# Kernel tuning notes

Hardware: AMD Instinct MI355X
Metric: run time of the kernel (lower is better)

The kernel has to match this reference:

```python
import jax, jax.numpy as jnp
import numpy as np


def setup_inputs() -> dict:
    key = jax.random.key(0)
    k1, k2 = jax.random.split(key)
    pred_m = jax.random.normal(k1, (64, 1, 512, 512), dtype=jnp.float32)
    # boxes: (x, y, s_x, s_y) per (batch, frame, target); values in [0, 256)
    multi_targets = jax.random.randint(k2, (64, 5, 32, 4), 0, 256, dtype=jnp.int32)
    return {"pred_m": pred_m, "multi_targets": multi_targets}


def _paint_heatmap(multi_targets, B, H, W, dtype):
    """Vectorized replacement for the triple-nested box-fill loop.

    Uses a 2D difference-array scatter + double cumsum: each box adds
    +1/-1 at its four corners; after prefix sums, count>0 marks painted
    pixels (original sets them to 255 regardless of overlap).
    """
    gt = multi_targets.reshape(B, -1, 4)  # [B, N, 4], N = n_frames*n_targets
    x, y, sx, sy = gt[..., 0], gt[..., 1], gt[..., 2], gt[..., 3]
    # python slicing clamps the end of the slice at H/W
    x1 = jnp.minimum(x, H)
    y1 = jnp.minimum(y, W)
    x2 = jnp.minimum(x + sx, H)
    y2 = jnp.minimum(y + sy, W)
    b_idx = jnp.broadcast_to(jnp.arange(B)[:, None], x.shape)
    diff = jnp.zeros((B, H + 1, W + 1), jnp.int32)
    diff = diff.at[b_idx, x1, y1].add(1)
    diff = diff.at[b_idx, x1, y2].add(-1)
    diff = diff.at[b_idx, x2, y1].add(-1)
    diff = diff.at[b_idx, x2, y2].add(1)
    count = jnp.cumsum(jnp.cumsum(diff, axis=1), axis=2)[:, :H, :W]
    return (count > 0).astype(dtype) * jnp.asarray(255.0, dtype)


def reference(pred_m, multi_targets):
    B, _, H, W = pred_m.shape
    heatmap = _paint_heatmap(multi_targets, B, H, W, pred_m.dtype)  # [B, H, W]
    target = heatmap[:, None]            # [B, 1, H, W]
    pred = jax.nn.sigmoid(pred_m)        # [B, 1, H, W]
    smooth = jnp.asarray(1.0, pred_m.dtype)
    intersection = jnp.sum(pred * target, axis=(1, 2, 3))
    pred_sum = jnp.sum(pred, axis=(1, 2, 3))
    target_sum = jnp.sum(target, axis=(1, 2, 3))
    loss = (intersection + smooth) / (pred_sum + target_sum - intersection + smooth)
    return 1.0 - jnp.mean(loss)
```

## Files before the change

### kernel.cpp

```cpp
#include <hip/hip_runtime.h>
#include <math.h>

#define SLICES 32
#define ROWS_PER_SLICE 16
#define NBOXES 160

static __device__ __forceinline__ float fast_sigmoid(float x) {
    return __builtin_amdgcn_rcpf(1.0f + __expf(-x));
}

__global__ __launch_bounds__(256) void mask_kernel(
    const int* __restrict__ targets, unsigned* __restrict__ gmask)
{
    __shared__ uint2 s_box[NBOXES];
    __shared__ int s_wcnt[4];

    const int t = threadIdx.x;
    const int slice = blockIdx.x;
    const int b = blockIdx.y;
    const int r0 = slice * ROWS_PER_SLICE;
    const int lane = t & 63, wave = t >> 6;

    bool keep = false;
    unsigned px = 0, py = 0;
    if (t < NBOXES) {
        const int4 g = ((const int4*)targets)[(size_t)b * NBOXES + t];
        int x1 = min(g.x, 512), y1 = min(g.y, 512);
        int x2 = min(g.x + g.z, 512), y2 = min(g.y + g.w, 512);
        int cx1 = max(x1, r0), cx2 = min(x2, r0 + ROWS_PER_SLICE);
        px = (unsigned)cx1 | ((unsigned)cx2 << 16);
        py = (unsigned)y1 | ((unsigned)y2 << 16);
        keep = (cx2 > cx1) && (y2 > y1);
    }
    const unsigned long long bal = __ballot(keep);
    if (lane == 0) s_wcnt[wave] = (int)__popcll(bal);
    __syncthreads();
    int wbase = 0;
    for (int w = 0; w < wave; ++w) wbase += s_wcnt[w];
    const int nb = s_wcnt[0] + s_wcnt[1] + s_wcnt[2] + s_wcnt[3];
    if (keep) {
        const int idx = wbase + (int)__popcll(bal & ((1ull << lane) - 1ull));
        s_box[idx] = make_uint2(px, py);
    }
    __syncthreads();

    const int r = r0 + (t >> 4);
    const unsigned wb = (unsigned)(t & 15) * 32u;
    unsigned m = 0;
#pragma unroll 2
    for (int k = 0; k < nb; ++k) {
        const uint2 bx = s_box[k];
        const int x1 = (int)(bx.x & 0xffffu), x2 = (int)(bx.x >> 16);
        const int y1 = (int)(bx.y & 0xffffu), y2 = (int)(bx.y >> 16);
        const bool in_row = (r >= x1) && (r < x2);
        int lo = max(y1, (int)wb), hi = min(y2, (int)wb + 32);
        int nn = hi - lo;
        unsigned bits = 0xFFFFFFFFu >> ((32 - nn) & 31);
        unsigned contrib = bits << ((unsigned)(lo - (int)wb) & 31u);
        m |= (in_row && nn > 0) ? contrib : 0u;
    }
    gmask[(size_t)b * 8192 + (size_t)r0 * 16 + t] = m;
}

__global__ __launch_bounds__(256, 4) void stream_kernel(
    const float* __restrict__ pred, const unsigned* __restrict__ gmask,
    float* __restrict__ partials)
{
    const int t = threadIdx.x;
    const int slice = blockIdx.x;
    const int b = blockIdx.y;
    const int r0 = slice * ROWS_PER_SLICE;
    const int lane = t & 63, wave = t >> 6;
    const int col4 = t & 127;
    const int rb = t >> 7;
    const int widx = col4 >> 3;
    const unsigned bb = (unsigned)(col4 & 7) * 4u;

    const unsigned* gm = gmask + (size_t)b * 8192 + (size_t)(r0 + rb) * 16 + widx;
    unsigned w0 = gm[0 * 32];
    unsigned w1 = gm[1 * 32];
    unsigned w2 = gm[2 * 32];
    unsigned w3 = gm[3 * 32];
    unsigned w4 = gm[4 * 32];
    unsigned w5 = gm[5 * 32];
    unsigned w6 = gm[6 * 32];
    unsigned w7 = gm[7 * 32];

    const float4* p4 = (const float4*)pred;
    const size_t g0 = (size_t)b * 65536 + (size_t)(r0 + rb) * 128 + col4;
    float4 v0 = p4[g0 + 0 * 256];
    float4 v1 = p4[g0 + 1 * 256];
    float4 v2 = p4[g0 + 2 * 256];
    float4 v3 = p4[g0 + 3 * 256];
    float4 v4 = p4[g0 + 4 * 256];
    float4 v5 = p4[g0 + 5 * 256];
    float4 v6 = p4[g0 + 6 * 256];
    float4 v7 = p4[g0 + 7 * 256];

    float psum = 0.0f, isum = 0.0f;
    int cnt = 0;
#define ACC(V, W)                                                       \
    {                                                                   \
        const unsigned n = ((W) >> bb) & 0xFu;                          \
        float s0 = fast_sigmoid((V).x);                                 \
        float s1 = fast_sigmoid((V).y);                                 \
        float s2 = fast_sigmoid((V).z);                                 \
        float s3 = fast_sigmoid((V).w);                                 \
        psum += (s0 + s1) + (s2 + s3);                                  \
        cnt += __popc(n);                                               \
        isum += ((n & 1u) ? s0 : 0.0f) + ((n & 2u) ? s1 : 0.0f)         \
              + ((n & 4u) ? s2 : 0.0f) + ((n & 8u) ? s3 : 0.0f);        \
    }
    ACC(v0, w0) ACC(v1, w1) ACC(v2, w2) ACC(v3, w3)
    ACC(v4, w4) ACC(v5, w5) ACC(v6, w6) ACC(v7, w7)
#undef ACC
    float csum = (float)cnt;

    for (int off = 32; off > 0; off >>= 1) {
        psum += __shfl_down(psum, off);
        isum += __shfl_down(isum, off);
        csum += __shfl_down(csum, off);
    }
    if (lane == 0) {
        float* o = partials + (((size_t)b * SLICES + slice) * 4 + wave) * 3;
        o[0] = psum; o[1] = isum; o[2] = csum;
    }
}

__global__ __launch_bounds__(64) void final_kernel(
    const float* __restrict__ partials, float* __restrict__ out)
{
    const int b = threadIdx.x;
    double P = 0, I = 0, C = 0;
    const float* p = partials + (size_t)b * SLICES * 4 * 3;
    for (int s = 0; s < SLICES * 4; ++s) {
        P += (double)p[s * 3 + 0];
        I += (double)p[s * 3 + 1];
        C += (double)p[s * 3 + 2];
    }
    const double inter = 255.0 * I;
    const double tsum  = 255.0 * C;
    double loss = (inter + 1.0) / (P + tsum - inter + 1.0);
    for (int off = 32; off > 0; off >>= 1) loss += __shfl_down(loss, off);
    if (b == 0) out[0] = (float)(1.0 - loss / 64.0);
}

extern "C" void kernel_launch(void* const* d_in, const int* in_sizes, int n_in,
                              void* d_out, int out_size, void* d_ws, size_t ws_size,
                              hipStream_t stream) {
    const float* pred    = (const float*)d_in[0];
    const int*   targets = (const int*)d_in[1];
    float* out = (float*)d_out;

    float* partials = (float*)d_ws;
    unsigned* gmask = (unsigned*)((char*)d_ws + (96 << 10));

    dim3 grid(SLICES, 64);
    mask_kernel<<<grid, 256, 0, stream>>>(targets, gmask);
    stream_kernel<<<grid, 256, 0, stream>>>(pred, gmask, partials);
    final_kernel<<<1, 64, 0, stream>>>(partials, out);
}
```

Measured before the change: 113.0 us.

## Fuse mask painting into streaming reduction with early inline-asm pred loads

Merges the mask-building kernel and the sigmoid reduction kernel into one launch. The mask is kept in shared memory instead of being written to and read back from global memory. The pred loads are issued through inline asm before the box processing, so their latency overlaps the mask computation, with an explicit s_waitcnt before use. Partials move to a structure-of-arrays layout so the final kernel can read them as float4. This removes one launch and a global round trip, but relies on hand-written waitcnt and asm loads that the compiler cannot track.

```diff
diff --git a/kernel.cpp b/kernel.cpp
--- a/kernel.cpp
+++ b/kernel.cpp
@@ -4,27 +4,46 @@
 #define SLICES 32
 #define ROWS_PER_SLICE 16
 #define NBOXES 160
+#define THREADS 256
 
 static __device__ __forceinline__ float fast_sigmoid(float x) {
     return __builtin_amdgcn_rcpf(1.0f + __expf(-x));
 }
 
-__global__ __launch_bounds__(256) void mask_kernel(
-    const int* __restrict__ targets, unsigned* __restrict__ gmask)
+__global__ __launch_bounds__(THREADS, 4) void paint_reduce_kernel(
+    const float* __restrict__ pred, const int* __restrict__ targets,
+    float* __restrict__ partials)
 {
-    __shared__ uint2 s_box[NBOXES];
-    __shared__ int s_wcnt[4];
+    __shared__ uint2 s_box[192];
+    __shared__ int s_wcnt[3];
+    __shared__ unsigned s_mask[256];
 
     const int t = threadIdx.x;
     const int slice = blockIdx.x;
     const int b = blockIdx.y;
     const int r0 = slice * ROWS_PER_SLICE;
     const int lane = t & 63, wave = t >> 6;
+    const int col4 = t & 127;
+    const int rb = t >> 7;
+
+    int4 g = make_int4(0, 0, 0, 0);
+    if (t < NBOXES) g = ((const int4*)targets)[(size_t)b * NBOXES + t];
+
+    const float4* p4 = (const float4*)pred + (size_t)b * 65536
+                     + (size_t)(r0 + rb) * 128 + col4;
+    float4 v0, v1, v2, v3, v4, v5, v6, v7;
+    asm volatile("global_load_dwordx4 %0, %1, off" : "=v"(v0) : "v"(p4 + 0 * 256));
+    asm volatile("global_load_dwordx4 %0, %1, off" : "=v"(v1) : "v"(p4 + 1 * 256));
+    asm volatile("global_load_dwordx4 %0, %1, off" : "=v"(v2) : "v"(p4 + 2 * 256));
+    asm volatile("global_load_dwordx4 %0, %1, off" : "=v"(v3) : "v"(p4 + 3 * 256));
+    asm volatile("global_load_dwordx4 %0, %1, off" : "=v"(v4) : "v"(p4 + 4 * 256));
+    asm volatile("global_load_dwordx4 %0, %1, off" : "=v"(v5) : "v"(p4 + 5 * 256));
+    asm volatile("global_load_dwordx4 %0, %1, off" : "=v"(v6) : "v"(p4 + 6 * 256));
+    asm volatile("global_load_dwordx4 %0, %1, off" : "=v"(v7) : "v"(p4 + 7 * 256));
 
     bool keep = false;
     unsigned px = 0, py = 0;
     if (t < NBOXES) {
-        const int4 g = ((const int4*)targets)[(size_t)b * NBOXES + t];
         int x1 = min(g.x, 512), y1 = min(g.y, 512);
         int x2 = min(g.x + g.z, 512), y2 = min(g.y + g.w, 512);
         int cx1 = max(x1, r0), cx2 = min(x2, r0 + ROWS_PER_SLICE);
@@ -33,69 +52,45 @@
         keep = (cx2 > cx1) && (y2 > y1);
     }
     const unsigned long long bal = __ballot(keep);
-    if (lane == 0) s_wcnt[wave] = (int)__popcll(bal);
-    __syncthreads();
-    int wbase = 0;
-    for (int w = 0; w < wave; ++w) wbase += s_wcnt[w];
-    const int nb = s_wcnt[0] + s_wcnt[1] + s_wcnt[2] + s_wcnt[3];
+    if (wave < 3 && lane == 0) s_wcnt[wave] = (int)__popcll(bal);
     if (keep) {
-        const int idx = wbase + (int)__popcll(bal & ((1ull << lane) - 1ull));
-        s_box[idx] = make_uint2(px, py);
+        const int idx = (int)__popcll(bal & ((1ull << lane) - 1ull));
+        s_box[wave * 64 + idx] = make_uint2(px, py);
     }
     __syncthreads();
 
     const int r = r0 + (t >> 4);
-    const unsigned wb = (unsigned)(t & 15) * 32u;
+    const int wbase = (t & 15) * 32;
     unsigned m = 0;
-#pragma unroll 2
-    for (int k = 0; k < nb; ++k) {
-        const uint2 bx = s_box[k];
-        const int x1 = (int)(bx.x & 0xffffu), x2 = (int)(bx.x >> 16);
-        const int y1 = (int)(bx.y & 0xffffu), y2 = (int)(bx.y >> 16);
-        const bool in_row = (r >= x1) && (r < x2);
-        int lo = max(y1, (int)wb), hi = min(y2, (int)wb + 32);
-        int nn = hi - lo;
-        unsigned bits = 0xFFFFFFFFu >> ((32 - nn) & 31);
-        unsigned contrib = bits << ((unsigned)(lo - (int)wb) & 31u);
-        m |= (in_row && nn > 0) ? contrib : 0u;
+    for (int w = 0; w < 3; ++w) {
+        const int nb = s_wcnt[w];
+        for (int k = 0; k < nb; ++k) {
+            const uint2 bx = s_box[w * 64 + k];
+            const int x1 = (int)(bx.x & 0xffffu), x2 = (int)(bx.x >> 16);
+            const int y1 = (int)(bx.y & 0xffffu), y2 = (int)(bx.y >> 16);
+            const bool in_row = (r >= x1) && (r < x2);
+            int lo = max(y1, wbase), hi = min(y2, wbase + 32);
+            int nn = hi - lo;
+            unsigned bits = 0xFFFFFFFFu >> ((32 - nn) & 31);
+            unsigned contrib = bits << ((unsigned)(lo - wbase) & 31u);
+            m |= (in_row && nn > 0) ? contrib : 0u;
+        }
     }
-    gmask[(size_t)b * 8192 + (size_t)r0 * 16 + t] = m;
-}
+    s_mask[t] = m;
+    __syncthreads();
 
-__global__ __launch_bounds__(256, 4) void stream_kernel(
-    const float* __restrict__ pred, const unsigned* __restrict__ gmask,
-    float* __restrict__ partials)
-{
-    const int t = threadIdx.x;
-    const int slice = blockIdx.x;
-    const int b = blockIdx.y;
-    const int r0 = slice * ROWS_PER_SLICE;
-    const int lane = t & 63, wave = t >> 6;
-    const int col4 = t & 127;
-    const int rb = t >> 7;
     const int widx = col4 >> 3;
     const unsigned bb = (unsigned)(col4 & 7) * 4u;
+    unsigned w0 = s_mask[(rb +  0) * 16 + widx];
+    unsigned w1 = s_mask[(rb +  2) * 16 + widx];
+    unsigned w2 = s_mask[(rb +  4) * 16 + widx];
+    unsigned w3 = s_mask[(rb +  6) * 16 + widx];
+    unsigned w4 = s_mask[(rb +  8) * 16 + widx];
+    unsigned w5 = s_mask[(rb + 10) * 16 + widx];
+    unsigned w6 = s_mask[(rb + 12) * 16 + widx];
+    unsigned w7 = s_mask[(rb + 14) * 16 + widx];
 
-    const unsigned* gm = gmask + (size_t)b * 8192 + (size_t)(r0 + rb) * 16 + widx;
-    unsigned w0 = gm[0 * 32];
-    unsigned w1 = gm[1 * 32];
-    unsigned w2 = gm[2 * 32];
-    unsigned w3 = gm[3 * 32];
-    unsigned w4 = gm[4 * 32];
-    unsigned w5 = gm[5 * 32];
-    unsigned w6 = gm[6 * 32];
-    unsigned w7 = gm[7 * 32];
-
-    const float4* p4 = (const float4*)pred;
-    const size_t g0 = (size_t)b * 65536 + (size_t)(r0 + rb) * 128 + col4;
-    float4 v0 = p4[g0 + 0 * 256];
-    float4 v1 = p4[g0 + 1 * 256];
-    float4 v2 = p4[g0 + 2 * 256];
-    float4 v3 = p4[g0 + 3 * 256];
-    float4 v4 = p4[g0 + 4 * 256];
-    float4 v5 = p4[g0 + 5 * 256];
-    float4 v6 = p4[g0 + 6 * 256];
-    float4 v7 = p4[g0 + 7 * 256];
+    asm volatile("s_waitcnt vmcnt(0)" ::: "memory");
 
     float psum = 0.0f, isum = 0.0f;
     int cnt = 0;
@@ -122,8 +117,10 @@
         csum += __shfl_down(csum, off);
     }
     if (lane == 0) {
-        float* o = partials + (((size_t)b * SLICES + slice) * 4 + wave) * 3;
-        o[0] = psum; o[1] = isum; o[2] = csum;
+        const size_t idx = ((size_t)b * SLICES + slice) * 4 + wave;
+        partials[idx]         = psum;
+        partials[8192 + idx]  = isum;
+        partials[16384 + idx] = csum;
     }
 }
 
@@ -131,12 +128,14 @@
     const float* __restrict__ partials, float* __restrict__ out)
 {
     const int b = threadIdx.x;
+    const float4* P4 = (const float4*)(partials)         + b * 32;
+    const float4* I4 = (const float4*)(partials + 8192)  + b * 32;
+    const float4* C4 = (const float4*)(partials + 16384) + b * 32;
     double P = 0, I = 0, C = 0;
-    const float* p = partials + (size_t)b * SLICES * 4 * 3;
-    for (int s = 0; s < SLICES * 4; ++s) {
-        P += (double)p[s * 3 + 0];
-        I += (double)p[s * 3 + 1];
-        C += (double)p[s * 3 + 2];
+    for (int j = 0; j < 32; ++j) {
+        float4 p = P4[j]; P += (double)p.x + p.y + p.z + p.w;
+        float4 i = I4[j]; I += (double)i.x + i.y + i.z + i.w;
+        float4 c = C4[j]; C += (double)c.x + c.y + c.z + c.w;
     }
     const double inter = 255.0 * I;
     const double tsum  = 255.0 * C;
@@ -151,12 +150,9 @@
     const float* pred    = (const float*)d_in[0];
     const int*   targets = (const int*)d_in[1];
     float* out = (float*)d_out;
-
     float* partials = (float*)d_ws;
-    unsigned* gmask = (unsigned*)((char*)d_ws + (96 << 10));
 
     dim3 grid(SLICES, 64);
-    mask_kernel<<<grid, 256, 0, stream>>>(targets, gmask);
-    stream_kernel<<<grid, 256, 0, stream>>>(pred, gmask, partials);
+    paint_reduce_kernel<<<grid, THREADS, 0, stream>>>(pred, targets, partials);
     final_kernel<<<1, 64, 0, stream>>>(partials, out);
 }
```

Result: faster. 108.8 us (-3.7%).
